# Optimization experiments

Measured on AMD Instinct MI355X. Metric: run time of the kernel, lower is better.

Reference implementation:

```python
import jax, jax.numpy as jnp
import numpy as np

N = 50000      # nodes
E = 800000     # edges (avg degree 16)
D_IN = 96
D_OUT = 96


def setup_inputs() -> dict:
    key = jax.random.key(0)
    k1, k2, k3, k4 = jax.random.split(key, 4)
    x = jax.random.normal(k1, (N, D_IN), dtype=jnp.float32)
    edge_index = jax.random.randint(k2, (2, E), 0, N, dtype=jnp.int32)
    scale = 1.0 / np.sqrt(D_IN)
    Wl = jax.random.normal(k3, (D_OUT, D_IN), dtype=jnp.float32) * scale  # lin_l weight (neighbors)
    bl = jnp.zeros((D_OUT,), dtype=jnp.float32)                           # lin_l bias
    Wr = jax.random.normal(k4, (D_OUT, D_IN), dtype=jnp.float32) * scale  # lin_r weight (root), no bias
    return {"x": x, "edge_index": edge_index, "Wl": Wl, "bl": bl, "Wr": Wr}


def reference(x, edge_index, Wl, bl, Wr):
    # SAGEConv (mean aggr): z = lin_l(mean_{j in N(i)} x_j) + lin_r(x_i), then ReLU.
    # Dropout p=0.0 -> identity.
    src, dst = edge_index[0], edge_index[1]  # messages flow src -> dst (PyG convention)
    msg = x[src]  # [E, D_IN] gather
    agg = jax.ops.segment_sum(msg, dst, num_segments=N)                     # [N, D_IN]
    deg = jax.ops.segment_sum(jnp.ones((E, 1), x.dtype), dst, num_segments=N)  # [N, 1]
    agg = agg / jnp.maximum(deg, 1.0)  # mean; isolated nodes -> 0
    z = agg @ Wl.T + bl + x @ Wr.T     # [N, D_OUT]
    return jax.nn.relu(z)
```

## Files before the change

kernel.cpp:

```cpp
#include <hip/hip_runtime.h>
#include <hip/hip_bf16.h>

#define D 96
#define CAP 32
#define OVF_MAX 65536
#define NB1 256
#define BUKSHIFT 8
#define CAPB 8192

typedef __attribute__((ext_vector_type(8))) short bf16x8;
typedef __attribute__((ext_vector_type(4))) float f32x4;
typedef unsigned u32x3 __attribute__((ext_vector_type(3), aligned(4)));

__device__ __forceinline__ short f2bf(float f)
{
    union { __hip_bfloat16 h; short s; } u;
    u.h = __float2bfloat16(f);
    return u.s;
}

__device__ __forceinline__ bf16x8 load_frag(const float* p)
{
    float4 lo = *(const float4*)p;
    float4 hi = *(const float4*)(p + 4);
    bf16x8 r;
    r[0] = f2bf(lo.x); r[1] = f2bf(lo.y); r[2] = f2bf(lo.z); r[3] = f2bf(lo.w);
    r[4] = f2bf(hi.x); r[5] = f2bf(hi.y); r[6] = f2bf(hi.z); r[7] = f2bf(hi.w);
    return r;
}

__device__ __forceinline__ float bf_lo(unsigned p) { return __uint_as_float(p << 16); }
__device__ __forceinline__ float bf_hi(unsigned p) { return __uint_as_float(p & 0xFFFF0000u); }

__global__ __launch_bounds__(256) void init_kernel(
    const float* __restrict__ Wl, const float* __restrict__ Wr,
    __hip_bfloat16* __restrict__ wbf, int* __restrict__ cnt, int N)
{
    const int idx = blockIdx.x * 256 + threadIdx.x;
    if (idx == 0) cnt[N] = 0;
    if (idx < 2304) {
        int mat = idx / 1152;
        int rem = idx - mat * 1152;
        int n  = rem / 12;
        int k8 = rem - n * 12;
        const float* Wp = mat ? Wr : Wl;
        bf16x8 v = load_frag(Wp + (size_t)n * D + k8 * 8);
        int ct = n >> 4, m = n & 15, kt = k8 >> 2, quad = k8 & 3;
        ((bf16x8*)wbf)[(mat * 18 + ct * 3 + kt) * 64 + quad * 16 + m] = v;
    }
}

__global__ __launch_bounds__(256) void p1_hist(
    const int* __restrict__ dst, int* __restrict__ hist, int nbuk, int E)
{
    __shared__ int h[256];
    for (int i = threadIdx.x; i < nbuk; i += 256) h[i] = 0;
    __syncthreads();
    const int CS = (E + NB1 - 1) / NB1;
    const int base = blockIdx.x * CS;
    int lim = E - base; if (lim > CS) lim = CS; if (lim < 0) lim = 0;
    for (int i = threadIdx.x; i < lim; i += 256)
        atomicAdd(&h[dst[base + i] >> BUKSHIFT], 1);
    __syncthreads();
    for (int i = threadIdx.x; i < nbuk; i += 256)
        hist[blockIdx.x * nbuk + i] = h[i];
}

__global__ __launch_bounds__(256) void kpre(
    const int* __restrict__ hist, int* __restrict__ ofs,
    int* __restrict__ tot, int nbuk)
{
    __shared__ int sc[256];
    const int bu = blockIdx.x, t = threadIdx.x;
    int v = hist[t * nbuk + bu];
    sc[t] = v;
    __syncthreads();
    #pragma unroll
    for (int off = 1; off < 256; off <<= 1) {
        int x = (t >= off) ? sc[t - off] : 0;
        __syncthreads();
        sc[t] += x;
        __syncthreads();
    }
    ofs[t * nbuk + bu] = bu * CAPB + (sc[t] - v);
    if (t == 255) tot[bu] = sc[t];
}

__global__ __launch_bounds__(256) void p2_gemm(
    const int* __restrict__ src, const int* __restrict__ dst,
    const int* __restrict__ ofs, unsigned* __restrict__ ebuf,
    const float* __restrict__ x, const __hip_bfloat16* __restrict__ wbf,
    __hip_bfloat16* __restrict__ hl, float* __restrict__ hr,
    int nbuk, int N, int E)
{
    if (blockIdx.x < NB1) {
        __shared__ int mo[256];
        for (int i = threadIdx.x; i < nbuk; i += 256)
            mo[i] = ofs[blockIdx.x * nbuk + i];
        __syncthreads();
        const int CS = (E + NB1 - 1) / NB1;
        const int base = blockIdx.x * CS;
        int lim = E - base; if (lim > CS) lim = CS; if (lim < 0) lim = 0;
        for (int i = threadIdx.x; i < lim; i += 256) {
            int e = base + i;
            int d = dst[e], s = src[e];
            int bu = d >> BUKSHIFT;
            int g = atomicAdd(&mo[bu], 1);
            if (g < (bu + 1) * CAPB)
                ebuf[g] = (unsigned)s | ((unsigned)(d & 255) << 16);
        }
        return;
    }

    const int gk = blockIdx.x - NB1;
    const int gwave = (gk * 256 + threadIdx.x) >> 6;
    const int nrt = N / 16;
    if (gwave >= nrt) return;
    const int lane = threadIdx.x & 63;
    const int m = lane & 15, quad = lane >> 4;
    const int row = gwave * 16 + m;
    const bf16x8* wb = (const bf16x8*)wbf;

    bf16x8 a[3];
    #pragma unroll
    for (int kt = 0; kt < 3; ++kt)
        a[kt] = load_frag(x + (size_t)row * D + kt * 32 + quad * 8);

    const int orow = gwave * 16 + quad * 4;
    #pragma unroll
    for (int ct = 0; ct < 6; ++ct) {
        f32x4 accl = {0.f, 0.f, 0.f, 0.f};
        f32x4 accr = {0.f, 0.f, 0.f, 0.f};
        #pragma unroll
        for (int kt = 0; kt < 3; ++kt)
            accl = __builtin_amdgcn_mfma_f32_16x16x32_bf16(
                a[kt], wb[(ct * 3 + kt) * 64 + lane], accl, 0, 0, 0);
        #pragma unroll
        for (int kt = 0; kt < 3; ++kt)
            accr = __builtin_amdgcn_mfma_f32_16x16x32_bf16(
                a[kt], wb[(18 + ct * 3 + kt) * 64 + lane], accr, 0, 0, 0);
        int col = ct * 16 + m;
        int sl = col / 24, c = col - sl * 24;
        #pragma unroll
        for (int r = 0; r < 4; ++r) {
            int node = orow + r;
            hl[((size_t)sl * N + node) * 32 + c] = __float2bfloat16(accl[r]);
            hr[(size_t)node * D + col] = accr[r];
        }
    }
}

__global__ __launch_bounds__(256) void p3_build(
    const unsigned* __restrict__ ebuf, const int* __restrict__ tot,
    int* __restrict__ cnt, unsigned short* __restrict__ slot,
    int* __restrict__ ovf, int N)
{
    __shared__ int cl[256];
    __shared__ unsigned short sl[256 * CAP];
    const int bu = blockIdx.x, t = threadIdx.x;
    cl[t] = 0;
    __syncthreads();
    const int n = tot[bu];
    const unsigned* eb = ebuf + (size_t)bu * CAPB;
    for (int i = t; i < n; i += 256) {
        unsigned e = eb[i];
        int dl = e >> 16, s = e & 0xFFFFu;
        int pos = atomicAdd(&cl[dl], 1);
        if (pos < CAP) {
            sl[dl * CAP + pos] = (unsigned short)s;
        } else {
            int o = atomicAdd(&cnt[N], 1);
            if (o < OVF_MAX) { ovf[2 * o] = (bu << BUKSHIFT) + dl; ovf[2 * o + 1] = s; }
        }
    }
    __syncthreads();
    const int node = (bu << BUKSHIFT) + t;
    if (node < N) cnt[node] = cl[t];
    const unsigned* slD = (const unsigned*)sl;
    unsigned* sg = (unsigned*)slot + (size_t)bu * 256 * 16;
    #pragma unroll
    for (int k = 0; k < 16; ++k) {
        int idx = k * 256 + t;
        if (((bu << BUKSHIFT) + (idx >> 4)) < N) sg[idx] = slD[idx];
    }
}

__global__ __launch_bounds__(256) void agg_kernel(
    const __hip_bfloat16* __restrict__ hl, const int* __restrict__ cnt,
    const unsigned short* __restrict__ slot, const int* __restrict__ ovf,
    const float* __restrict__ bl, float* __restrict__ out, int N)
{
    const int lane = threadIdx.x & 63;
    const int wv = threadIdx.x >> 6;
    const int xcd = blockIdx.x & 7;
    const int s  = xcd >> 1;
    const int sb = ((blockIdx.x >> 3) << 1) | (xcd & 1);
    if (sb >= 3125) return;
    const int n0 = sb * 16 + wv * 4;
    const int nn = lane >> 4;
    const int e4 = (lane >> 2) & 3;
    const int r  = lane & 3;
    const int n  = n0 + nn;

    const int deg = cnt[n];
    const int dcm = min(deg, CAP);
    const unsigned* slotD = (const unsigned*)slot;
    unsigned sid = slotD[(size_t)n0 * 16 + lane];
    int um = dcm;
    um = max(um, __shfl_xor(um, 16));
    um = max(um, __shfl_xor(um, 32));

    const unsigned short* hs = (const unsigned short*)hl + (size_t)s * N * 32;
    float a0 = 0.f, a1 = 0.f, a2 = 0.f, a3 = 0.f, a4 = 0.f, a5 = 0.f;
    #pragma unroll 2
    for (int j = 0; j < um; j += 4) {
        int idx = j + e4;
        unsigned dw = __shfl(sid, nn * 16 + (idx >> 1));
        bool act = idx < dcm;
        int nb = act ? ((idx & 1) ? (int)(dw >> 16) : (int)(dw & 0xFFFFu)) : 0;
        u32x3 p = *(const u32x3*)((const char*)hs + (size_t)nb * 64 + r * 12);
        float mk = act ? 1.f : 0.f;
        a0 += mk * bf_lo(p.x); a1 += mk * bf_hi(p.x);
        a2 += mk * bf_lo(p.y); a3 += mk * bf_hi(p.y);
        a4 += mk * bf_lo(p.z); a5 += mk * bf_hi(p.z);
    }
    #pragma unroll
    for (int off = 4; off <= 8; off <<= 1) {
        a0 += __shfl_xor(a0, off); a1 += __shfl_xor(a1, off);
        a2 += __shfl_xor(a2, off); a3 += __shfl_xor(a3, off);
        a4 += __shfl_xor(a4, off); a5 += __shfl_xor(a5, off);
    }
    if (e4 == 0) {
        int ovfn = min(cnt[N], OVF_MAX);
        if (ovfn) {
            for (int k = 0; k < ovfn; ++k) {
                if (ovf[2 * k] == n) {
                    int nb = ovf[2 * k + 1];
                    u32x3 p = *(const u32x3*)((const char*)hs + (size_t)nb * 64 + r * 12);
                    a0 += bf_lo(p.x); a1 += bf_hi(p.x);
                    a2 += bf_lo(p.y); a3 += bf_hi(p.y);
                    a4 += bf_lo(p.z); a5 += bf_hi(p.z);
                }
            }
        }
        const int o = s * 24 + r * 6;
        float inv = 1.0f / fmaxf((float)deg, 1.0f);
        float* op = out + (size_t)n * D + o;
        float2 u0 = *(const float2*)op;
        float2 u1 = *(const float2*)(op + 2);
        float2 u2 = *(const float2*)(op + 4);
        u0.x = fmaxf(a0 * inv + bl[o]     + u0.x, 0.f);
        u0.y = fmaxf(a1 * inv + bl[o + 1] + u0.y, 0.f);
        u1.x = fmaxf(a2 * inv + bl[o + 2] + u1.x, 0.f);
        u1.y = fmaxf(a3 * inv + bl[o + 3] + u1.y, 0.f);
        u2.x = fmaxf(a4 * inv + bl[o + 4] + u2.x, 0.f);
        u2.y = fmaxf(a5 * inv + bl[o + 5] + u2.y, 0.f);
        *(float2*)op       = u0;
        *(float2*)(op + 2) = u1;
        *(float2*)(op + 4) = u2;
    }
}

extern "C" void kernel_launch(void* const* d_in, const int* in_sizes, int n_in,
                              void* d_out, int out_size, void* d_ws, size_t ws_size,
                              hipStream_t stream)
{
    const float* x  = (const float*)d_in[0];
    const int*   ei = (const int*)d_in[1];
    const float* Wl = (const float*)d_in[2];
    const float* bl = (const float*)d_in[3];
    const float* Wr = (const float*)d_in[4];
    float* out = (float*)d_out;

    const int N = in_sizes[0] / D;
    const int E = in_sizes[1] / 2;
    const int* src = ei;
    const int* dst = ei + E;
    const int nbuk = (N + 255) >> BUKSHIFT;

    char* p = (char*)d_ws;
    __hip_bfloat16* wbf = (__hip_bfloat16*)p;          p += 36864;
    __hip_bfloat16* hl  = (__hip_bfloat16*)p;          p += (size_t)4 * N * 32 * 2;
    unsigned short* slot = (unsigned short*)p;         p += (size_t)N * CAP * 2;
    int* cnt = (int*)p;                                p += ((size_t)(N + 1) * 4 + 255) / 256 * 256;
    int* ovf = (int*)p;                                p += (size_t)2 * OVF_MAX * 4;
    int* hist = (int*)p;                               p += (size_t)NB1 * nbuk * 4;
    int* ofs = (int*)p;                                p += (size_t)NB1 * nbuk * 4;
    int* tot = (int*)p;                                p += ((size_t)nbuk * 4 + 255) / 256 * 256;
    unsigned* ebuf = (unsigned*)p;

    init_kernel<<<9, 256, 0, stream>>>(Wl, Wr, wbf, cnt, N);
    p1_hist<<<NB1, 256, 0, stream>>>(dst, hist, nbuk, E);
    kpre<<<nbuk, 256, 0, stream>>>(hist, ofs, tot, nbuk);

    const int nrt = N / 16;
    const int gemmb = (nrt + 3) / 4;
    p2_gemm<<<NB1 + gemmb, 256, 0, stream>>>(
        src, dst, ofs, ebuf, x, wbf, hl, out, nbuk, N, E);

    p3_build<<<nbuk, 256, 0, stream>>>(ebuf, tot, cnt, slot, ovf, N);

    agg_kernel<<<12504, 256, 0, stream>>>(hl, cnt, slot, ovf, bl, out, N);
}
```

Measured before the change: 152.3 us.

## Fuse slot build with aggregation and fold prefix scan into scatter

Shrinks destination buckets from 256 to 64 nodes and fuses the slot-table build with the mean aggregation, so neighbor lists stay in shared memory instead of going through a global slot/count/overflow round trip. The separate prefix-scan kernel is dropped: each scatter block sums the histograms of earlier blocks itself. Weight conversion is merged into the histogram launch. Together this cuts the pipeline from six launches to three. In exchange, aggregation runs on only about 782 blocks that each loop over 16 node groups, which lowers parallelism. Overflow is now capped per bucket at 256 entries in shared memory, and the redundant serial prefix sums in the scatter blocks add extra reads.

New measurement: 190.5 us. +25.1%, slower.

```diff
diff --git a/kernel.cpp b/kernel.cpp
--- a/kernel.cpp
+++ b/kernel.cpp
@@ -3,10 +3,12 @@
 
 #define D 96
 #define CAP 32
-#define OVF_MAX 65536
 #define NB1 256
-#define BUKSHIFT 8
-#define CAPB 8192
+#define BUKSHIFT 6
+#define BUKN 64
+#define CAPB 2048
+#define NBUK_MAX 1024
+#define OVL_MAX 256
 
 typedef __attribute__((ext_vector_type(8))) short bf16x8;
 typedef __attribute__((ext_vector_type(4))) float f32x4;
@@ -32,28 +34,26 @@
 __device__ __forceinline__ float bf_lo(unsigned p) { return __uint_as_float(p << 16); }
 __device__ __forceinline__ float bf_hi(unsigned p) { return __uint_as_float(p & 0xFFFF0000u); }
 
-__global__ __launch_bounds__(256) void init_kernel(
-    const float* __restrict__ Wl, const float* __restrict__ Wr,
-    __hip_bfloat16* __restrict__ wbf, int* __restrict__ cnt, int N)
-{
-    const int idx = blockIdx.x * 256 + threadIdx.x;
-    if (idx == 0) cnt[N] = 0;
-    if (idx < 2304) {
-        int mat = idx / 1152;
-        int rem = idx - mat * 1152;
-        int n  = rem / 12;
-        int k8 = rem - n * 12;
-        const float* Wp = mat ? Wr : Wl;
-        bf16x8 v = load_frag(Wp + (size_t)n * D + k8 * 8);
-        int ct = n >> 4, m = n & 15, kt = k8 >> 2, quad = k8 & 3;
-        ((bf16x8*)wbf)[(mat * 18 + ct * 3 + kt) * 64 + quad * 16 + m] = v;
-    }
-}
-
-__global__ __launch_bounds__(256) void p1_hist(
-    const int* __restrict__ dst, int* __restrict__ hist, int nbuk, int E)
-{
-    __shared__ int h[256];
+__global__ __launch_bounds__(256) void init_hist(
+    const int* __restrict__ dst, const float* __restrict__ Wl,
+    const float* __restrict__ Wr, __hip_bfloat16* __restrict__ wbf,
+    int* __restrict__ hist, int nbuk, int E)
+{
+    if (blockIdx.x >= NB1) {
+        int idx = (blockIdx.x - NB1) * 256 + threadIdx.x;
+        if (idx < 2304) {
+            int mat = idx / 1152;
+            int rem = idx - mat * 1152;
+            int n  = rem / 12;
+            int k8 = rem - n * 12;
+            const float* Wp = mat ? Wr : Wl;
+            bf16x8 v = load_frag(Wp + (size_t)n * D + k8 * 8);
+            int ct = n >> 4, m = n & 15, kt = k8 >> 2, quad = k8 & 3;
+            ((bf16x8*)wbf)[(mat * 18 + ct * 3 + kt) * 64 + quad * 16 + m] = v;
+        }
+        return;
+    }
+    __shared__ int h[NBUK_MAX];
     for (int i = threadIdx.x; i < nbuk; i += 256) h[i] = 0;
     __syncthreads();
     const int CS = (E + NB1 - 1) / NB1;
@@ -66,40 +66,27 @@
         hist[blockIdx.x * nbuk + i] = h[i];
 }
 
-__global__ __launch_bounds__(256) void kpre(
-    const int* __restrict__ hist, int* __restrict__ ofs,
-    int* __restrict__ tot, int nbuk)
-{
-    __shared__ int sc[256];
-    const int bu = blockIdx.x, t = threadIdx.x;
-    int v = hist[t * nbuk + bu];
-    sc[t] = v;
-    __syncthreads();
-    #pragma unroll
-    for (int off = 1; off < 256; off <<= 1) {
-        int x = (t >= off) ? sc[t - off] : 0;
-        __syncthreads();
-        sc[t] += x;
-        __syncthreads();
-    }
-    ofs[t * nbuk + bu] = bu * CAPB + (sc[t] - v);
-    if (t == 255) tot[bu] = sc[t];
-}
-
 __global__ __launch_bounds__(256) void p2_gemm(
     const int* __restrict__ src, const int* __restrict__ dst,
-    const int* __restrict__ ofs, unsigned* __restrict__ ebuf,
+    const int* __restrict__ hist, int* __restrict__ tot,
+    unsigned* __restrict__ ebuf,
     const float* __restrict__ x, const __hip_bfloat16* __restrict__ wbf,
     __hip_bfloat16* __restrict__ hl, float* __restrict__ hr,
     int nbuk, int N, int E)
 {
     if (blockIdx.x < NB1) {
-        __shared__ int mo[256];
-        for (int i = threadIdx.x; i < nbuk; i += 256)
-            mo[i] = ofs[blockIdx.x * nbuk + i];
+        __shared__ int mo[NBUK_MAX];
+        const int blk = blockIdx.x;
+        for (int t = threadIdx.x; t < nbuk; t += 256) {
+            int acc = 0;
+            #pragma unroll 4
+            for (int b = 0; b < blk; ++b) acc += hist[b * nbuk + t];
+            mo[t] = t * CAPB + acc;
+            if (blk == NB1 - 1) tot[t] = acc + hist[(NB1 - 1) * nbuk + t];
+        }
         __syncthreads();
         const int CS = (E + NB1 - 1) / NB1;
-        const int base = blockIdx.x * CS;
+        const int base = blk * CS;
         int lim = E - base; if (lim > CS) lim = CS; if (lim < 0) lim = 0;
         for (int i = threadIdx.x; i < lim; i += 256) {
             int e = base + i;
@@ -107,7 +94,7 @@
             int bu = d >> BUKSHIFT;
             int g = atomicAdd(&mo[bu], 1);
             if (g < (bu + 1) * CAPB)
-                ebuf[g] = (unsigned)s | ((unsigned)(d & 255) << 16);
+                ebuf[g] = (unsigned)s | ((unsigned)(d & (BUKN - 1)) << 16);
         }
         return;
     }
@@ -150,114 +137,99 @@
     }
 }
 
-__global__ __launch_bounds__(256) void p3_build(
+__global__ __launch_bounds__(256) void p3agg(
     const unsigned* __restrict__ ebuf, const int* __restrict__ tot,
-    int* __restrict__ cnt, unsigned short* __restrict__ slot,
-    int* __restrict__ ovf, int N)
-{
-    __shared__ int cl[256];
-    __shared__ unsigned short sl[256 * CAP];
+    const __hip_bfloat16* __restrict__ hl, const float* __restrict__ bl,
+    float* __restrict__ out, int nbuk, int N)
+{
+    __shared__ int cl[BUKN];
+    __shared__ unsigned short sl[BUKN * CAP];
+    __shared__ unsigned ovl[OVL_MAX];
+    __shared__ int ovc;
     const int bu = blockIdx.x, t = threadIdx.x;
-    cl[t] = 0;
-    __syncthreads();
+    if (t < BUKN) cl[t] = 0;
+    if (t == 0) ovc = 0;
+    __syncthreads();
+
     const int n = tot[bu];
     const unsigned* eb = ebuf + (size_t)bu * CAPB;
     for (int i = t; i < n; i += 256) {
         unsigned e = eb[i];
-        int dl = e >> 16, s = e & 0xFFFFu;
+        int dl = e >> 16, s = (int)(e & 0xFFFFu);
         int pos = atomicAdd(&cl[dl], 1);
         if (pos < CAP) {
             sl[dl * CAP + pos] = (unsigned short)s;
         } else {
-            int o = atomicAdd(&cnt[N], 1);
-            if (o < OVF_MAX) { ovf[2 * o] = (bu << BUKSHIFT) + dl; ovf[2 * o + 1] = s; }
-        }
-    }
-    __syncthreads();
-    const int node = (bu << BUKSHIFT) + t;
-    if (node < N) cnt[node] = cl[t];
-    const unsigned* slD = (const unsigned*)sl;
-    unsigned* sg = (unsigned*)slot + (size_t)bu * 256 * 16;
-    #pragma unroll
-    for (int k = 0; k < 16; ++k) {
-        int idx = k * 256 + t;
-        if (((bu << BUKSHIFT) + (idx >> 4)) < N) sg[idx] = slD[idx];
-    }
-}
-
-__global__ __launch_bounds__(256) void agg_kernel(
-    const __hip_bfloat16* __restrict__ hl, const int* __restrict__ cnt,
-    const unsigned short* __restrict__ slot, const int* __restrict__ ovf,
-    const float* __restrict__ bl, float* __restrict__ out, int N)
-{
-    const int lane = threadIdx.x & 63;
-    const int wv = threadIdx.x >> 6;
-    const int xcd = blockIdx.x & 7;
-    const int s  = xcd >> 1;
-    const int sb = ((blockIdx.x >> 3) << 1) | (xcd & 1);
-    if (sb >= 3125) return;
-    const int n0 = sb * 16 + wv * 4;
+            int o = atomicAdd(&ovc, 1);
+            if (o < OVL_MAX) ovl[o] = e;
+        }
+    }
+    __syncthreads();
+
+    const int wv = t >> 6, lane = t & 63;
     const int nn = lane >> 4;
     const int e4 = (lane >> 2) & 3;
     const int r  = lane & 3;
-    const int n  = n0 + nn;
-
-    const int deg = cnt[n];
-    const int dcm = min(deg, CAP);
-    const unsigned* slotD = (const unsigned*)slot;
-    unsigned sid = slotD[(size_t)n0 * 16 + lane];
-    int um = dcm;
-    um = max(um, __shfl_xor(um, 16));
-    um = max(um, __shfl_xor(um, 32));
-
-    const unsigned short* hs = (const unsigned short*)hl + (size_t)s * N * 32;
-    float a0 = 0.f, a1 = 0.f, a2 = 0.f, a3 = 0.f, a4 = 0.f, a5 = 0.f;
-    #pragma unroll 2
-    for (int j = 0; j < um; j += 4) {
-        int idx = j + e4;
-        unsigned dw = __shfl(sid, nn * 16 + (idx >> 1));
-        bool act = idx < dcm;
-        int nb = act ? ((idx & 1) ? (int)(dw >> 16) : (int)(dw & 0xFFFFu)) : 0;
-        u32x3 p = *(const u32x3*)((const char*)hs + (size_t)nb * 64 + r * 12);
-        float mk = act ? 1.f : 0.f;
-        a0 += mk * bf_lo(p.x); a1 += mk * bf_hi(p.x);
-        a2 += mk * bf_lo(p.y); a3 += mk * bf_hi(p.y);
-        a4 += mk * bf_lo(p.z); a5 += mk * bf_hi(p.z);
-    }
-    #pragma unroll
-    for (int off = 4; off <= 8; off <<= 1) {
-        a0 += __shfl_xor(a0, off); a1 += __shfl_xor(a1, off);
-        a2 += __shfl_xor(a2, off); a3 += __shfl_xor(a3, off);
-        a4 += __shfl_xor(a4, off); a5 += __shfl_xor(a5, off);
-    }
-    if (e4 == 0) {
-        int ovfn = min(cnt[N], OVF_MAX);
-        if (ovfn) {
-            for (int k = 0; k < ovfn; ++k) {
-                if (ovf[2 * k] == n) {
-                    int nb = ovf[2 * k + 1];
-                    u32x3 p = *(const u32x3*)((const char*)hs + (size_t)nb * 64 + r * 12);
-                    a0 += bf_lo(p.x); a1 += bf_hi(p.x);
-                    a2 += bf_lo(p.y); a3 += bf_hi(p.y);
-                    a4 += bf_lo(p.z); a5 += bf_hi(p.z);
+    const unsigned short* hs = (const unsigned short*)hl + (size_t)wv * N * 32;
+    const int o = wv * 24 + r * 6;
+    const float b0 = bl[o],     b1 = bl[o + 1], b2 = bl[o + 2];
+    const float b3 = bl[o + 3], b4 = bl[o + 4], b5 = bl[o + 5];
+    const int novc = min(ovc, OVL_MAX);
+
+    for (int q = 0; q < 16; ++q) {
+        const int nq = q * 4;
+        const int deg = cl[nq + nn];
+        const int dcm = min(deg, CAP);
+        int um = max(max(cl[nq], cl[nq + 1]), max(cl[nq + 2], cl[nq + 3]));
+        um = min(um, CAP);
+
+        float a0 = 0.f, a1 = 0.f, a2 = 0.f, a3 = 0.f, a4 = 0.f, a5 = 0.f;
+        #pragma unroll 2
+        for (int j = 0; j < um; j += 4) {
+            int idx = j + e4;
+            bool act = idx < dcm;
+            int nb = act ? (int)sl[(nq + nn) * CAP + idx] : 0;
+            u32x3 p = *(const u32x3*)((const char*)hs + (size_t)nb * 64 + r * 12);
+            float mk = act ? 1.f : 0.f;
+            a0 += mk * bf_lo(p.x); a1 += mk * bf_hi(p.x);
+            a2 += mk * bf_lo(p.y); a3 += mk * bf_hi(p.y);
+            a4 += mk * bf_lo(p.z); a5 += mk * bf_hi(p.z);
+        }
+        #pragma unroll
+        for (int off = 4; off <= 8; off <<= 1) {
+            a0 += __shfl_xor(a0, off); a1 += __shfl_xor(a1, off);
+            a2 += __shfl_xor(a2, off); a3 += __shfl_xor(a3, off);
+            a4 += __shfl_xor(a4, off); a5 += __shfl_xor(a5, off);
+        }
+        if (e4 == 0) {
+            const int node = (bu << BUKSHIFT) + nq + nn;
+            if (node < N) {
+                for (int k = 0; k < novc; ++k) {
+                    unsigned e = ovl[k];
+                    if ((int)(e >> 16) == nq + nn) {
+                        int nb = (int)(e & 0xFFFFu);
+                        u32x3 p = *(const u32x3*)((const char*)hs + (size_t)nb * 64 + r * 12);
+                        a0 += bf_lo(p.x); a1 += bf_hi(p.x);
+                        a2 += bf_lo(p.y); a3 += bf_hi(p.y);
+                        a4 += bf_lo(p.z); a5 += bf_hi(p.z);
+                    }
                 }
+                const float inv = 1.0f / fmaxf((float)deg, 1.0f);
+                float* op = out + (size_t)node * D + o;
+                float2 u0 = *(const float2*)op;
+                float2 u1 = *(const float2*)(op + 2);
+                float2 u2 = *(const float2*)(op + 4);
+                u0.x = fmaxf(a0 * inv + b0 + u0.x, 0.f);
+                u0.y = fmaxf(a1 * inv + b1 + u0.y, 0.f);
+                u1.x = fmaxf(a2 * inv + b2 + u1.x, 0.f);
+                u1.y = fmaxf(a3 * inv + b3 + u1.y, 0.f);
+                u2.x = fmaxf(a4 * inv + b4 + u2.x, 0.f);
+                u2.y = fmaxf(a5 * inv + b5 + u2.y, 0.f);
+                *(float2*)op       = u0;
+                *(float2*)(op + 2) = u1;
+                *(float2*)(op + 4) = u2;
             }
         }
-        const int o = s * 24 + r * 6;
-        float inv = 1.0f / fmaxf((float)deg, 1.0f);
-        float* op = out + (size_t)n * D + o;
-        float2 u0 = *(const float2*)op;
-        float2 u1 = *(const float2*)(op + 2);
-        float2 u2 = *(const float2*)(op + 4);
-        u0.x = fmaxf(a0 * inv + bl[o]     + u0.x, 0.f);
-        u0.y = fmaxf(a1 * inv + bl[o + 1] + u0.y, 0.f);
-        u1.x = fmaxf(a2 * inv + bl[o + 2] + u1.x, 0.f);
-        u1.y = fmaxf(a3 * inv + bl[o + 3] + u1.y, 0.f);
-        u2.x = fmaxf(a4 * inv + bl[o + 4] + u2.x, 0.f);
-        u2.y = fmaxf(a5 * inv + bl[o + 5] + u2.y, 0.f);
-        *(float2*)op       = u0;
-        *(float2*)(op + 2) = u1;
-        *(float2*)(op + 4) = u2;
     }
 }
 
@@ -276,29 +248,21 @@
     const int E = in_sizes[1] / 2;
     const int* src = ei;
     const int* dst = ei + E;
-    const int nbuk = (N + 255) >> BUKSHIFT;
+    const int nbuk = (N + BUKN - 1) >> BUKSHIFT;
 
     char* p = (char*)d_ws;
-    __hip_bfloat16* wbf = (__hip_bfloat16*)p;          p += 36864;
-    __hip_bfloat16* hl  = (__hip_bfloat16*)p;          p += (size_t)4 * N * 32 * 2;
-    unsigned short* slot = (unsigned short*)p;         p += (size_t)N * CAP * 2;
-    int* cnt = (int*)p;                                p += ((size_t)(N + 1) * 4 + 255) / 256 * 256;
-    int* ovf = (int*)p;                                p += (size_t)2 * OVF_MAX * 4;
-    int* hist = (int*)p;                               p += (size_t)NB1 * nbuk * 4;
-    int* ofs = (int*)p;                                p += (size_t)NB1 * nbuk * 4;
-    int* tot = (int*)p;                                p += ((size_t)nbuk * 4 + 255) / 256 * 256;
+    __hip_bfloat16* wbf = (__hip_bfloat16*)p;    p += 36864;
+    __hip_bfloat16* hl  = (__hip_bfloat16*)p;    p += (size_t)4 * N * 32 * 2;
+    int* hist = (int*)p;                         p += ((size_t)NB1 * nbuk * 4 + 255) / 256 * 256;
+    int* tot = (int*)p;                          p += ((size_t)nbuk * 4 + 255) / 256 * 256;
     unsigned* ebuf = (unsigned*)p;
 
-    init_kernel<<<9, 256, 0, stream>>>(Wl, Wr, wbf, cnt, N);
-    p1_hist<<<NB1, 256, 0, stream>>>(dst, hist, nbuk, E);
-    kpre<<<nbuk, 256, 0, stream>>>(hist, ofs, tot, nbuk);
+    init_hist<<<NB1 + 9, 256, 0, stream>>>(dst, Wl, Wr, wbf, hist, nbuk, E);
 
     const int nrt = N / 16;
     const int gemmb = (nrt + 3) / 4;
     p2_gemm<<<NB1 + gemmb, 256, 0, stream>>>(
-        src, dst, ofs, ebuf, x, wbf, hl, out, nbuk, N, E);
-
-    p3_build<<<nbuk, 256, 0, stream>>>(ebuf, tot, cnt, slot, ovf, N);
-
-    agg_kernel<<<12504, 256, 0, stream>>>(hl, cnt, slot, ovf, bl, out, N);
-}
+        src, dst, hist, tot, ebuf, x, wbf, hl, out, nbuk, N, E);
+
+    p3agg<<<nbuk, 256, 0, stream>>>(ebuf, tot, hl, bl, out, nbuk, N);
+}
```
